# Kernel tuning notes

Measured on AMD Instinct MI355X. Metric: run time of the kernel, lower is better.

Reference implementation:

```python
import jax, jax.numpy as jnp
import numpy as np

NEG_BIG = -9e15

def setup_inputs() -> dict:
    key = jax.random.key(0)
    kx, ka, kW, k1, k2 = jax.random.split(key, 5)
    B, N, F, H, D = 8, 1024, 1024, 16, 64
    x = jax.random.normal(kx, (B, N, F), dtype=jnp.float32)
    adj = jax.random.randint(ka, (B, N, N), 0, 2, dtype=jnp.int32)
    # xavier_uniform with gain=1.414
    gain = 1.414
    limW = gain * np.sqrt(6.0 / (F + D))
    lima = gain * np.sqrt(6.0 / (D + 1))
    W = jax.random.uniform(kW, (H, F, D), minval=-limW, maxval=limW, dtype=jnp.float32)
    a1 = jax.random.uniform(k1, (H, D), minval=-lima, maxval=lima, dtype=jnp.float32)
    a2 = jax.random.uniform(k2, (H, D), minval=-lima, maxval=lima, dtype=jnp.float32)
    return {"x": x, "adj": adj, "W": W, "a1": a1, "a2": a2}

def reference(x, adj, W, a1, a2):
    alpha = 0.2
    # Wh: [B, H, N, D]
    Wh = jnp.einsum('bnf,hfd->bhnd', x, W)
    f1 = jnp.einsum('bhnd,hd->bhn', Wh, a1)  # [B,H,N]
    f2 = jnp.einsum('bhnd,hd->bhn', Wh, a2)  # [B,H,N]
    e = f1[:, :, :, None] + f2[:, :, None, :]          # [B,H,N,N]
    e = jnp.where(e > 0, e, alpha * e)                  # leaky relu
    mask = (adj > 0)[:, None, :, :]                     # [B,1,N,N]
    scores = jnp.where(mask, e, NEG_BIG)
    attn = jax.nn.softmax(scores, axis=-1)              # [B,H,N,N]
    # dropout omitted (inference / training=False)
    h_prime = jnp.einsum('bhnm,bhmd->bhnd', attn, Wh)   # [B,H,N,D]
    B, H, N, D = h_prime.shape
    # concat heads along feature dim (matches torch.cat over dim=2)
    y = jnp.transpose(h_prime, (0, 2, 1, 3)).reshape(B, N, H * D)
    return y
```

## Files before the change

kernel.cpp:

```cpp
#include <hip/hip_runtime.h>
#include <hip/hip_bf16.h>

typedef float    f32x4 __attribute__((ext_vector_type(4)));
typedef short    s16x8 __attribute__((ext_vector_type(8)));
typedef _Float16 f16x8 __attribute__((ext_vector_type(8)));
typedef _Float16 f16x4 __attribute__((ext_vector_type(4)));
typedef unsigned int   u32x4 __attribute__((ext_vector_type(4)));


__device__ __forceinline__ unsigned short bf16rne(float f){
  unsigned u = __float_as_uint(f);
  return (unsigned short)((u + 0x7FFFu + ((u >> 16) & 1u)) >> 16);
}

__global__ __launch_bounds__(256) void prepw_kernel(const float* __restrict__ W,
    unsigned short* __restrict__ Wt)
{
  const int tx = threadIdx.x & 15, ty = threadIdx.x >> 4;
  const int f0 = blockIdx.x * 16, d0 = blockIdx.y * 16, hh = blockIdx.z;
  __shared__ float t[16][17];
  t[ty][tx] = W[(size_t)hh * 65536 + (size_t)(f0 + ty) * 64 + (d0 + tx)];
  __syncthreads();
  float v = t[tx][ty];
  size_t o = (size_t)(hh * 64 + d0 + ty) * 1024 + (f0 + tx);
  Wt[o] = bf16rne(v);
}

__global__ __launch_bounds__(256) void adjmask_kernel(const int* __restrict__ adj,
    unsigned* __restrict__ maskb)
{
  const int lane = threadIdx.x & 63;
  int gw = (blockIdx.x * 256 + threadIdx.x) >> 6;
  for (int s = gw; s < 131072; s += 4096) {
    int a = adj[(size_t)s * 64 + lane];
    unsigned long long m = __ballot(a > 0);
    if (lane == 0) {
      maskb[s * 2]     = (unsigned)m;
      maskb[s * 2 + 1] = (unsigned)(m >> 32);
    }
  }
}

__global__ __launch_bounds__(256, 3) void gemm_kernel(const float* __restrict__ x,
    const unsigned short* __restrict__ Btg,
    const float* __restrict__ a1, const float* __restrict__ a2,
    _Float16* __restrict__ WhT, float* __restrict__ f1, float* __restrict__ f2)
{
  __shared__ unsigned short Ah[128 * 40], Bh[128 * 40];
  const int tid  = threadIdx.x;
  const int lane = tid & 63, wave = tid >> 6;
  const int m0 = blockIdx.x * 128, n0 = blockIdx.y * 128;
  const int wm = (wave & 1) * 64, wn = (wave >> 1) * 64;
  const int rA = lane & 15, kg = lane >> 4;

  f32x4 acc[4][4] = {};

  for (int k0 = 0; k0 < 1024; k0 += 32) {
#pragma unroll
    for (int r = 0; r < 4; ++r) {
      int flat = r * 256 + tid;
      int row = flat >> 3;
      int c4  = (flat & 7) << 2;
      f32x4 v = *reinterpret_cast<const f32x4*>(&x[(size_t)(m0 + row) * 1024 + k0 + c4]);
      uint2 pk;
      __hip_bfloat162 t0 = __float22bfloat162_rn(make_float2(v[0], v[1]));
      __hip_bfloat162 t1 = __float22bfloat162_rn(make_float2(v[2], v[3]));
      __builtin_memcpy(&pk.x, &t0, 4);
      __builtin_memcpy(&pk.y, &t1, 4);
      *reinterpret_cast<uint2*>(&Ah[row * 40 + c4]) = pk;
    }
#pragma unroll
    for (int r = 0; r < 2; ++r) {
      int flat = r * 256 + tid;
      int row = flat >> 2;
      int o8  = (flat & 3) << 3;
      *reinterpret_cast<u32x4*>(&Bh[row * 40 + o8]) =
          *reinterpret_cast<const u32x4*>(&Btg[(size_t)(n0 + row) * 1024 + k0 + o8]);
    }
    __syncthreads();

    s16x8 ah[4], bh[4];
#pragma unroll
    for (int i = 0; i < 4; ++i)
      ah[i] = *reinterpret_cast<const s16x8*>(&Ah[(wm + i * 16 + rA) * 40 + kg * 8]);
#pragma unroll
    for (int j = 0; j < 4; ++j)
      bh[j] = *reinterpret_cast<const s16x8*>(&Bh[(wn + j * 16 + rA) * 40 + kg * 8]);
#pragma unroll
    for (int i = 0; i < 4; ++i)
#pragma unroll
      for (int j = 0; j < 4; ++j)
        acc[i][j] = __builtin_amdgcn_mfma_f32_16x16x32_bf16(ah[i], bh[j], acc[i][j], 0, 0, 0);
    __syncthreads();
  }

#pragma unroll
  for (int i = 0; i < 4; ++i) {
    int gm0 = m0 + wm + i * 16 + kg * 4;
#pragma unroll
    for (int j = 0; j < 4; ++j) {
      int gn = n0 + wn + j * 16 + rA;
      int bb = gm0 >> 10, nn = gm0 & 1023;
      int hh = gn >> 6,  dd = gn & 63;
      f16x4 hv;
#pragma unroll
      for (int jj = 0; jj < 4; ++jj) hv[jj] = (_Float16)acc[i][j][jj];
      *reinterpret_cast<f16x4*>(&WhT[((size_t)((bb * 16 + hh) * 64 + dd) << 10) + nn]) = hv;
    }
  }

  const int hw = (n0 + wn) >> 6;
  float a1v[4], a2v[4];
#pragma unroll
  for (int j = 0; j < 4; ++j) {
    int d = j * 16 + rA;
    a1v[j] = a1[hw * 64 + d];
    a2v[j] = a2[hw * 64 + d];
  }
#pragma unroll
  for (int i = 0; i < 4; ++i) {
#pragma unroll
    for (int jj = 0; jj < 4; ++jj) {
      float s1 = 0.f, s2 = 0.f;
#pragma unroll
      for (int j = 0; j < 4; ++j) {
        float v = acc[i][j][jj];
        s1 += v * a1v[j];
        s2 += v * a2v[j];
      }
#pragma unroll
      for (int off = 1; off < 16; off <<= 1) {
        s1 += __shfl_xor(s1, off);
        s2 += __shfl_xor(s2, off);
      }
      if (rA == 0) {
        int gm = m0 + wm + i * 16 + kg * 4 + jj;
        int bb = gm >> 10, nn = gm & 1023;
        size_t o = (size_t)(bb * 16 + hw) * 1024 + nn;
        f1[o] = s1;
        f2[o] = s2;
      }
    }
  }
}

__global__ __launch_bounds__(256, 4) void pv_kernel(const _Float16* __restrict__ WhT,
    const float* __restrict__ f1, const float* __restrict__ f2,
    const unsigned* __restrict__ maskb, float* __restrict__ y)
{
  const int tid = threadIdx.x, lane = tid & 63, wave = tid >> 6;
  const int rb = blockIdx.x, h = blockIdx.y, b = blockIdx.z;
  const int bh = b * 16 + h;
  const int n0 = rb * 64;
  const _Float16* whtb = WhT + ((size_t)bh << 16);

  __shared__ _Float16 Bsh[64 * 72];
  __shared__ float Cs[1024], Ds[1024];
  __shared__ float smx[4];
  __shared__ float rowR[64];

  const float K = 1.44269504f;

  float pmax;
  {
    f32x4 fv = *reinterpret_cast<const f32x4*>(&f2[(size_t)bh * 1024 + tid * 4]);
    f32x4 sv, cv, dv;
#pragma unroll
    for (int e = 0; e < 4; ++e) {
      sv[e] = fv[e] * K;
      cv[e] = __builtin_amdgcn_exp2f(sv[e]);
      dv[e] = __builtin_amdgcn_exp2f(0.2f * sv[e]);
    }
    *reinterpret_cast<f32x4*>(&Cs[tid * 4]) = cv;
    *reinterpret_cast<f32x4*>(&Ds[tid * 4]) = dv;
    pmax = fmaxf(fmaxf(sv[0], sv[1]), fmaxf(sv[2], sv[3]));
  }
#pragma unroll
  for (int off = 32; off; off >>= 1) pmax = fmaxf(pmax, __shfl_xor(pmax, off));
  if (lane == 0) smx[wave] = pmax;
  __syncthreads();

  const float m2s = fmaxf(fmaxf(smx[0], smx[1]), fmaxf(smx[2], smx[3]));

  const int rA = lane & 15, kg = lane >> 4;
  const int wrow = wave * 16;
  f32x4 acc[4] = {};
  const int rloc = wrow + rA;
  float At, Bt, den = 0.f;
  {
    float f1p = f1[(size_t)bh * 1024 + n0 + rloc] * K;
    float sf = f1p + m2s;
    float Mp = fmaxf(sf, 0.2f * sf);
    At = __builtin_amdgcn_exp2f(f1p - Mp);
    Bt = __builtin_amdgcn_exp2f(0.2f * f1p - Mp);
  }
  const unsigned* mrow = maskb + ((size_t)(b << 10) + n0 + rloc) * 32;

  for (int m0 = 0; m0 < 1024; m0 += 64) {
    uint2 mw2 = *reinterpret_cast<const uint2*>(&mrow[m0 >> 5]);
#pragma unroll
    for (int r = 0; r < 2; ++r) {
      int flat = r * 256 + tid;
      int d = flat >> 3, o = (flat & 7) << 3;
      *reinterpret_cast<u32x4*>(&Bsh[d * 72 + o]) =
          *reinterpret_cast<const u32x4*>(&whtb[(size_t)d * 1024 + m0 + o]);
    }
    __syncthreads();
#pragma unroll
    for (int ks = 0; ks < 2; ++ks) {
      const int kc = m0 + ks * 32 + kg * 8;
      f32x4 ca = *reinterpret_cast<const f32x4*>(&Cs[kc]);
      f32x4 cb = *reinterpret_cast<const f32x4*>(&Cs[kc + 4]);
      f32x4 da = *reinterpret_cast<const f32x4*>(&Ds[kc]);
      f32x4 db = *reinterpret_cast<const f32x4*>(&Ds[kc + 4]);
      unsigned mw = (&mw2.x)[ks] >> (kg * 8);
      f16x8 pa;
#pragma unroll
      for (int jj = 0; jj < 8; ++jj) {
        float C = (jj < 4) ? ca[jj] : cb[jj - 4];
        float D = (jj < 4) ? da[jj] : db[jj - 4];
        float p = fmaxf(At * C, Bt * D);
        p = ((mw >> jj) & 1u) ? p : 0.0f;
        den += p;
        pa[jj] = (_Float16)p;
      }
#pragma unroll
      for (int j = 0; j < 4; ++j) {
        f16x8 bf = *reinterpret_cast<const f16x8*>(&Bsh[(j * 16 + rA) * 72 + ks * 32 + kg * 8]);
        acc[j] = __builtin_amdgcn_mfma_f32_16x16x32_f16(pa, bf, acc[j], 0, 0, 0);
      }
    }
    __syncthreads();
  }

  den += __shfl_xor(den, 16);
  den += __shfl_xor(den, 32);
  if (kg == 0) rowR[rloc] = den > 0.f ? 1.0f / den : 0.f;
  __syncthreads();

#pragma unroll
  for (int j = 0; j < 4; ++j) {
#pragma unroll
    for (int jj = 0; jj < 4; ++jj) {
      int row = wrow + kg * 4 + jj;
      int n = n0 + row, d = j * 16 + rA;
      y[(((size_t)b * 1024 + n) << 10) + h * 64 + d] = acc[j][jj] * rowR[row];
    }
  }
}

extern "C" void kernel_launch(void* const* d_in, const int* in_sizes, int n_in,
                              void* d_out, int out_size, void* d_ws, size_t ws_size,
                              hipStream_t stream)
{
  const float* x  = (const float*)d_in[0];
  const int*   adj = (const int*)d_in[1];
  const float* W  = (const float*)d_in[2];
  const float* a1 = (const float*)d_in[3];
  const float* a2 = (const float*)d_in[4];
  float* y = (float*)d_out;

  char* ws = (char*)d_ws;
  unsigned short* Wt = (unsigned short*)(ws);
  unsigned*       maskb = (unsigned*)(ws + ((size_t)2 << 20));
  float* f1   = (float*)(ws + ((size_t)3 << 20));
  float* f2   = (float*)(ws + ((size_t)3 << 20) + ((size_t)512 << 10));
  _Float16* WhT = (_Float16*)(ws + ((size_t)4 << 20));

  prepw_kernel<<<dim3(64, 4, 16), 256, 0, stream>>>(W, Wt);
  adjmask_kernel<<<1024, 256, 0, stream>>>(adj, maskb);
  gemm_kernel<<<dim3(64, 8), 256, 0, stream>>>(x, Wt, a1, a2, WhT, f1, f2);
  pv_kernel<<<dim3(16, 16, 8), 256, 0, stream>>>(WhT, f1, f2, maskb, y);
}
```

Baseline: 106.6 us.

## Pre-convert x to bf16 in a fused prep kernel and merge prep launches

Merges the W-transpose and adjacency-bitmask kernels into a single prep kernel that also converts x to bf16 in workspace. The GEMM then loads bf16 x directly instead of loading fp32 x and converting it in every one of the 8 column-tile blocks, which cuts redundant global reads and conversion ALU work. One kernel launch is also removed. In exchange there is an extra full pass that writes and re-reads a 16 MB bf16 copy of x. The workspace must also be large enough to hold it at offset 20 MB.

```diff
diff --git a/kernel.cpp b/kernel.cpp
--- a/kernel.cpp
+++ b/kernel.cpp
@@ -1,5 +1,4 @@
 #include <hip/hip_runtime.h>
-#include <hip/hip_bf16.h>
 
 typedef float    f32x4 __attribute__((ext_vector_type(4)));
 typedef short    s16x8 __attribute__((ext_vector_type(8)));
@@ -13,35 +12,47 @@
   return (unsigned short)((u + 0x7FFFu + ((u >> 16) & 1u)) >> 16);
 }
 
-__global__ __launch_bounds__(256) void prepw_kernel(const float* __restrict__ W,
+__global__ __launch_bounds__(256) void prep_kernel(const int* __restrict__ adj,
+    const float* __restrict__ x, const float* __restrict__ W,
+    unsigned* __restrict__ maskb, unsigned short* __restrict__ xb,
     unsigned short* __restrict__ Wt)
 {
-  const int tx = threadIdx.x & 15, ty = threadIdx.x >> 4;
-  const int f0 = blockIdx.x * 16, d0 = blockIdx.y * 16, hh = blockIdx.z;
-  __shared__ float t[16][17];
-  t[ty][tx] = W[(size_t)hh * 65536 + (size_t)(f0 + ty) * 64 + (d0 + tx)];
-  __syncthreads();
-  float v = t[tx][ty];
-  size_t o = (size_t)(hh * 64 + d0 + ty) * 1024 + (f0 + tx);
-  Wt[o] = bf16rne(v);
-}
-
-__global__ __launch_bounds__(256) void adjmask_kernel(const int* __restrict__ adj,
-    unsigned* __restrict__ maskb)
-{
-  const int lane = threadIdx.x & 63;
-  int gw = (blockIdx.x * 256 + threadIdx.x) >> 6;
-  for (int s = gw; s < 131072; s += 4096) {
-    int a = adj[(size_t)s * 64 + lane];
-    unsigned long long m = __ballot(a > 0);
-    if (lane == 0) {
-      maskb[s * 2]     = (unsigned)m;
-      maskb[s * 2 + 1] = (unsigned)(m >> 32);
-    }
-  }
-}
-
-__global__ __launch_bounds__(256, 3) void gemm_kernel(const float* __restrict__ x,
+  const int bid = blockIdx.x, tid = threadIdx.x;
+  if (bid < 1024) {
+    const int lane = tid & 63;
+    int gw = (bid * 256 + tid) >> 6;
+    for (int s = gw; s < 131072; s += 4096) {
+      int a = adj[(size_t)s * 64 + lane];
+      unsigned long long m = __ballot(a > 0);
+      if (lane == 0) {
+        maskb[s * 2]     = (unsigned)m;
+        maskb[s * 2 + 1] = (unsigned)(m >> 32);
+      }
+    }
+  } else if (bid < 5120) {
+    int idx = ((bid - 1024) * 256 + tid) * 8;
+    f32x4 v0 = *reinterpret_cast<const f32x4*>(&x[idx]);
+    f32x4 v1 = *reinterpret_cast<const f32x4*>(&x[idx + 4]);
+    u32x4 o;
+    o[0] = (unsigned)bf16rne(v0[0]) | ((unsigned)bf16rne(v0[1]) << 16);
+    o[1] = (unsigned)bf16rne(v0[2]) | ((unsigned)bf16rne(v0[3]) << 16);
+    o[2] = (unsigned)bf16rne(v1[0]) | ((unsigned)bf16rne(v1[1]) << 16);
+    o[3] = (unsigned)bf16rne(v1[2]) | ((unsigned)bf16rne(v1[3]) << 16);
+    *reinterpret_cast<u32x4*>(&xb[idx]) = o;
+  } else {
+    __shared__ float t[16][17];
+    int rel = bid - 5120;
+    int f0 = (rel & 63) * 16, d0 = ((rel >> 6) & 3) * 16, hh = rel >> 8;
+    const int tx = tid & 15, ty = tid >> 4;
+    t[ty][tx] = W[(size_t)hh * 65536 + (size_t)(f0 + ty) * 64 + (d0 + tx)];
+    __syncthreads();
+    float v = t[tx][ty];
+    size_t o = (size_t)(hh * 64 + d0 + ty) * 1024 + (f0 + tx);
+    Wt[o] = bf16rne(v);
+  }
+}
+
+__global__ __launch_bounds__(256, 3) void gemm_kernel(const unsigned short* __restrict__ xb,
     const unsigned short* __restrict__ Btg,
     const float* __restrict__ a1, const float* __restrict__ a2,
     _Float16* __restrict__ WhT, float* __restrict__ f1, float* __restrict__ f2)
@@ -57,17 +68,12 @@
 
   for (int k0 = 0; k0 < 1024; k0 += 32) {
 #pragma unroll
-    for (int r = 0; r < 4; ++r) {
+    for (int r = 0; r < 2; ++r) {
       int flat = r * 256 + tid;
-      int row = flat >> 3;
-      int c4  = (flat & 7) << 2;
-      f32x4 v = *reinterpret_cast<const f32x4*>(&x[(size_t)(m0 + row) * 1024 + k0 + c4]);
-      uint2 pk;
-      __hip_bfloat162 t0 = __float22bfloat162_rn(make_float2(v[0], v[1]));
-      __hip_bfloat162 t1 = __float22bfloat162_rn(make_float2(v[2], v[3]));
-      __builtin_memcpy(&pk.x, &t0, 4);
-      __builtin_memcpy(&pk.y, &t1, 4);
-      *reinterpret_cast<uint2*>(&Ah[row * 40 + c4]) = pk;
+      int row = flat >> 2;
+      int o8  = (flat & 3) << 3;
+      *reinterpret_cast<u32x4*>(&Ah[row * 40 + o8]) =
+          *reinterpret_cast<const u32x4*>(&xb[(size_t)(m0 + row) * 1024 + k0 + o8]);
     }
 #pragma unroll
     for (int r = 0; r < 2; ++r) {
@@ -266,9 +272,9 @@
   float* f1   = (float*)(ws + ((size_t)3 << 20));
   float* f2   = (float*)(ws + ((size_t)3 << 20) + ((size_t)512 << 10));
   _Float16* WhT = (_Float16*)(ws + ((size_t)4 << 20));
-
-  prepw_kernel<<<dim3(64, 4, 16), 256, 0, stream>>>(W, Wt);
-  adjmask_kernel<<<1024, 256, 0, stream>>>(adj, maskb);
-  gemm_kernel<<<dim3(64, 8), 256, 0, stream>>>(x, Wt, a1, a2, WhT, f1, f2);
+  unsigned short* xb = (unsigned short*)(ws + ((size_t)20 << 20));
+
+  prep_kernel<<<9216, 256, 0, stream>>>(adj, x, W, maskb, xb, Wt);
+  gemm_kernel<<<dim3(64, 8), 256, 0, stream>>>(xb, Wt, a1, a2, WhT, f1, f2);
   pv_kernel<<<dim3(16, 16, 8), 256, 0, stream>>>(WhT, f1, f2, maskb, y);
 }
```

Measured after the change: 99.91 us. 1.07x faster.
